# Kernel tuning notes

Measured on AMD Instinct MI355X. Metric: run time of the kernel, lower is better.

Reference implementation:

```python
import jax, jax.numpy as jnp
import numpy as np

B, T, U, H = 4, 256, 64, 512
INNER, VOCAB = 512, 1024


def setup_inputs() -> dict:
    key = jax.random.key(0)
    ks = jax.random.split(key, 6)
    s_in = 1.0 / np.sqrt(2 * H)
    s_h = 1.0 / np.sqrt(INNER)
    return {
        "enc_state": jax.random.normal(ks[0], (B, T, H), dtype=jnp.float32),
        "dec_state": jax.random.normal(ks[1], (B, U, H), dtype=jnp.float32),
        "W1": jax.random.normal(ks[2], (2 * H, INNER), dtype=jnp.float32) * s_in,
        "b1": jnp.zeros((INNER,), dtype=jnp.float32),
        "W2": jax.random.normal(ks[3], (INNER, VOCAB), dtype=jnp.float32) * s_h,
        "b2": jnp.zeros((VOCAB,), dtype=jnp.float32),
    }


def reference(enc_state, dec_state, W1, b1, W2, b2):
    # JointNet: broadcast enc [B,T,1,H] and dec [B,1,U,H], concat -> Linear -> tanh -> Linear -> log_softmax
    # concat+Linear is split into two smaller matmuls (mathematically identical):
    # cat([e,d]) @ W1 == e @ W1[:H] + d @ W1[H:]
    enc_proj = jnp.einsum("bth,hi->bti", enc_state, W1[:H])      # [B,T,INNER]
    dec_proj = jnp.einsum("buh,hi->bui", dec_state, W1[H:])      # [B,U,INNER]
    hidden = jnp.tanh(enc_proj[:, :, None, :] + dec_proj[:, None, :, :] + b1)  # [B,T,U,INNER]
    logits = jnp.einsum("btui,iv->btuv", hidden, W2) + b2        # [B,T,U,VOCAB]
    return jax.nn.log_softmax(logits, axis=-1)
```

## Files before the change

### kernel.cpp

```cpp
#include <hip/hip_runtime.h>
#include <hip/hip_bf16.h>
#include <cstdint>
#include <cstddef>


typedef __attribute__((ext_vector_type(4))) float f32x4;

#define BS_CHUNK 32768

#define WS_EP_OFF 0
#define WS_DP_OFF (1024 * 512 * 4)
#define WS_W2_OFF (WS_DP_OFF + 256 * 512 * 4)

#define ASTRIDE 528
#define LDS_EP 33792
#define LDS_B0 36864
#define LDS_B1 69632
#define SMEM_TOTAL 102400

__device__ __forceinline__ unsigned short f2bf(float x) {
  unsigned int u = __builtin_bit_cast(unsigned int, x);
  u += 0x7FFFu + ((u >> 16) & 1u);
  return (unsigned short)(u >> 16);
}

__device__ __forceinline__ float fast_tanh(float x) {
  float ax = fabsf(x);
  float e = __expf(-2.0f * ax);
  float t = (1.0f - e) * __builtin_amdgcn_rcpf(1.0f + e);
  return copysignf(t, x);
}

#if __has_builtin(__builtin_amdgcn_cvt_pk_fp8_f32)
__device__ __forceinline__ unsigned int f2fp8x4(float a, float b, float c, float d) {
  unsigned int w = 0;
  w = (unsigned int)__builtin_amdgcn_cvt_pk_fp8_f32(a, b, (int)w, false);
  w = (unsigned int)__builtin_amdgcn_cvt_pk_fp8_f32(c, d, (int)w, true);
  return w;
}
#else
__device__ __forceinline__ unsigned int enc_e4m3(float x) {
  unsigned int u = __builtin_bit_cast(unsigned int, x);
  unsigned int s = (u >> 24) & 0x80u;
  float ax = fabsf(x);
  if (!(ax < 448.0f)) return s | 0x7Eu;
  if (ax < 0.0009765625f) return s;
  int e; float fr = frexpf(ax, &e);
  int E = e + 6;
  if (E >= 1) {
    unsigned int m = (unsigned int)rintf(fr * 16.0f);
    if (m == 16u) { m = 8u; E += 1; }
    if (E >= 16) return s | 0x7Eu;
    return s | ((unsigned int)E << 3) | (m - 8u);
  } else {
    unsigned int m = (unsigned int)rintf(ax * 512.0f);
    if (m >= 8u) return s | 0x08u;
    return s | m;
  }
}
__device__ __forceinline__ unsigned int f2fp8x4(float a, float b, float c, float d) {
  return enc_e4m3(a) | (enc_e4m3(b) << 8) | (enc_e4m3(c) << 16) | (enc_e4m3(d) << 24);
}
#endif

__global__ __launch_bounds__(512) void prep(
    const float* __restrict__ enc, const float* __restrict__ dec,
    const float* __restrict__ W1, const float* __restrict__ b1,
    const float* __restrict__ W2,
    float* __restrict__ ep, float* __restrict__ dp, char* __restrict__ w8st) {
  __shared__ float As[8 * 512];
  const int tid = threadIdx.x;
  if (blockIdx.x < 160) {
    const int r0 = blockIdx.x * 8;
    const bool isenc = (r0 < 1024);
    const float* A = isenc ? (enc + (size_t)r0 * 512) : (dec + (size_t)(r0 - 1024) * 512);
    const float* W = isenc ? W1 : (W1 + 512 * 512);
    float* O = isenc ? (ep + (size_t)r0 * 512) : (dp + (size_t)(r0 - 1024) * 512);

    for (int idx = tid; idx < 8 * 512; idx += 512) As[idx] = A[idx];
    __syncthreads();

    const int c = tid;
    float acc[8];
#pragma unroll
    for (int r = 0; r < 8; ++r) acc[r] = 0.0f;
    const float4* As4 = (const float4*)As;
#pragma unroll 2
    for (int k4 = 0; k4 < 128; ++k4) {
      const int kb = k4 * 4;
      float w0 = W[(size_t)(kb + 0) * 512 + c];
      float w1 = W[(size_t)(kb + 1) * 512 + c];
      float w2 = W[(size_t)(kb + 2) * 512 + c];
      float w3 = W[(size_t)(kb + 3) * 512 + c];
#pragma unroll
      for (int r = 0; r < 8; ++r) {
        float4 a = As4[r * 128 + k4];
        acc[r] += a.x * w0 + a.y * w1 + a.z * w2 + a.w * w3;
      }
    }
    const float bias = isenc ? b1[c] : 0.0f;
#pragma unroll
    for (int r = 0; r < 8; ++r) O[(size_t)r * 512 + c] = acc[r] + bias;
  } else {
    const int g = (blockIdx.x - 160) * 512 + tid;
    const int v = g & 1023;
    const int kc = g >> 10;
    const int s = (v >> 2) & 3;
    unsigned long long* dst =
        (unsigned long long*)(w8st + (size_t)kc * BS_CHUNK + (size_t)v * 32);
#pragma unroll
    for (int q = 0; q < 4; ++q) {
      float f[8];
#pragma unroll
      for (int j = 0; j < 8; ++j)
        f[j] = W2[(size_t)(kc * 32 + q * 8 + j) * 1024 + v];
      unsigned int lo = f2fp8x4(f[0], f[1], f[2], f[3]);
      unsigned int hi = f2fp8x4(f[4], f[5], f[6], f[7]);
      dst[q ^ s] = (unsigned long long)lo | ((unsigned long long)hi << 32);
    }
  }
}

__device__ __forceinline__ void stage32(const char* __restrict__ src, char* dst,
                                        int wave, int lane) {
  const int off = wave * 2048 + lane * 16;
#pragma unroll
  for (int j = 0; j < 2; ++j)
    __builtin_amdgcn_global_load_lds(
        (const __attribute__((address_space(1))) unsigned int*)(src + off + j * 1024),
        (__attribute__((address_space(3))) unsigned int*)(dst + off + j * 1024), 16, 0, 0);
}

__global__ __launch_bounds__(1024, 4) void joint(
    const float* __restrict__ ep, const float* __restrict__ dp,
    const char* __restrict__ w8st, const float* __restrict__ b2,
    float* __restrict__ out) {
  extern __shared__ char smem[];
  char* Asm = smem;
  float* epL = (float*)(smem + LDS_EP);
  char* Bs0 = smem + LDS_B0;
  char* Bs1 = smem + LDS_B1;
  float* redM = (float*)(smem + LDS_B0);
  float* redF = redM + 1024;
  float* redS = redF + 64;
  float* redF2 = redS + 1024;

  const int tid = threadIdx.x;
  const int wave = tid >> 6, lane = tid & 63;
  const int lo = lane & 15, hi = lane >> 4;
  const int bt = blockIdx.x;
  const int m0 = bt * 64;
  const int dprow0 = (bt >> 8) * 64;
  const int nbase = wave * 64;
  const int krot = bt & 15;

  float b2v[4];
#pragma unroll
  for (int ni = 0; ni < 4; ++ni) b2v[ni] = b2[nbase + ni * 16 + lo];

  stage32(w8st + (size_t)krot * BS_CHUNK, Bs0, wave, lane);
  stage32(w8st + (size_t)((krot + 1) & 15) * BS_CHUNK, Bs1, wave, lane);

  if (tid < 128) ((float4*)epL)[tid] = ((const float4*)(ep + (size_t)bt * 512))[tid];

  const int arow = tid & 63;
  const int c0 = (tid >> 6) * 32;
  float d[32];
  {
    const float* dpr = dp + (size_t)(dprow0 + arow) * 512 + c0;
#pragma unroll
    for (int j = 0; j < 8; ++j) *(float4*)(d + j * 4) = ((const float4*)dpr)[j];
  }
  __syncthreads();

  {
    unsigned int w8[8];
#pragma unroll
    for (int q = 0; q < 8; ++q) {
      float h0 = fast_tanh(epL[c0 + q * 4 + 0] + d[q * 4 + 0]);
      float h1 = fast_tanh(epL[c0 + q * 4 + 1] + d[q * 4 + 1]);
      float h2 = fast_tanh(epL[c0 + q * 4 + 2] + d[q * 4 + 2]);
      float h3 = fast_tanh(epL[c0 + q * 4 + 3] + d[q * 4 + 3]);
      w8[q] = f2fp8x4(h0, h1, h2, h3);
    }
    uint4* aw = (uint4*)(Asm + arow * ASTRIDE + c0);
    aw[0] = *(const uint4*)(w8);
    aw[1] = *(const uint4*)(w8 + 4);
  }

  f32x4 acc[4][4];
#pragma unroll
  for (int mi = 0; mi < 4; ++mi)
#pragma unroll
    for (int ni = 0; ni < 4; ++ni)
#pragma unroll
      for (int j = 0; j < 4; ++j) acc[mi][ni][j] = 0.0f;

  asm volatile("s_waitcnt lgkmcnt(0)" ::: "memory");
  __builtin_amdgcn_s_barrier();
  __builtin_amdgcn_sched_barrier(0);

  const int bswz = (hi * 8) ^ (((lo >> 2) & 3) << 3);

#define K_ITER(I, RD)                                                            \
  {                                                                              \
    const int i_ = (I);                                                          \
    if (i_ >= 14) asm volatile("s_waitcnt vmcnt(0)" ::: "memory");               \
    else          asm volatile("s_waitcnt vmcnt(2)" ::: "memory");               \
    __builtin_amdgcn_s_barrier();             \
    __builtin_amdgcn_sched_barrier(0);                                           \
    const int gc = (i_ + krot) & 15;                                             \
    unsigned long long a[4], b[4];                                               \
    _Pragma("unroll")                                                            \
    for (int ni = 0; ni < 4; ++ni)                                               \
      b[ni] = *(const unsigned long long*)(RD + (size_t)(nbase + ni * 16 + lo) * 32 + bswz); \
    _Pragma("unroll")                                                            \
    for (int mi = 0; mi < 4; ++mi)                                               \
      a[mi] = *(const unsigned long long*)(Asm + (size_t)(mi * 16 + lo) * ASTRIDE + gc * 32 + hi * 8); \
    asm volatile("s_waitcnt lgkmcnt(0)" ::: "memory");                           \
    __builtin_amdgcn_sched_barrier(0);                                           \
    __builtin_amdgcn_s_barrier();                 \
    __builtin_amdgcn_sched_barrier(0);                                           \
    if (i_ < 14)                                                                 \
      stage32(w8st + (size_t)(((i_ + 2 + krot) & 15)) * BS_CHUNK, RD, wave, lane); \
    __builtin_amdgcn_s_setprio(1);                                               \
    _Pragma("unroll")                                                            \
    for (int ni = 0; ni < 4; ++ni)                                               \
      _Pragma("unroll")                                                          \
      for (int mi = 0; mi < 4; ++mi)                                             \
        acc[mi][ni] = __builtin_amdgcn_mfma_f32_16x16x32_fp8_fp8(                \
            (long)a[mi], (long)b[ni], acc[mi][ni], 0, 0, 0);                     \
    __builtin_amdgcn_s_setprio(0);                                               \
  }

#pragma unroll 1
  for (int i2 = 0; i2 < 8; ++i2) {
    K_ITER(i2 * 2, Bs0);
    K_ITER(i2 * 2 + 1, Bs1);
  }
#undef K_ITER

#pragma unroll
  for (int mi = 0; mi < 4; ++mi)
#pragma unroll
    for (int ni = 0; ni < 4; ++ni)
#pragma unroll
      for (int j = 0; j < 4; ++j) acc[mi][ni][j] += b2v[ni];

  float pm[4][4];
#pragma unroll
  for (int mi = 0; mi < 4; ++mi)
#pragma unroll
    for (int r = 0; r < 4; ++r)
      pm[mi][r] = fmaxf(fmaxf(acc[mi][0][r], acc[mi][1][r]),
                        fmaxf(acc[mi][2][r], acc[mi][3][r]));
#pragma unroll
  for (int off = 1; off < 16; off <<= 1)
#pragma unroll
    for (int mi = 0; mi < 4; ++mi)
#pragma unroll
      for (int r = 0; r < 4; ++r)
        pm[mi][r] = fmaxf(pm[mi][r], __shfl_xor(pm[mi][r], off));
  if (lo == 0) {
#pragma unroll
    for (int mi = 0; mi < 4; ++mi)
#pragma unroll
      for (int r = 0; r < 4; ++r)
        redM[wave * 64 + mi * 16 + hi * 4 + r] = pm[mi][r];
  }
  asm volatile("s_waitcnt lgkmcnt(0)" ::: "memory");
  __builtin_amdgcn_s_barrier();
  {
    const int rr = tid >> 4, w = tid & 15;
    float v = redM[w * 64 + rr];
#pragma unroll
    for (int off = 1; off < 16; off <<= 1) v = fmaxf(v, __shfl_xor(v, off));
    if (w == 0) redF[rr] = v;
  }
  asm volatile("s_waitcnt lgkmcnt(0)" ::: "memory");
  __builtin_amdgcn_s_barrier();
  float rm[4][4];
#pragma unroll
  for (int mi = 0; mi < 4; ++mi)
#pragma unroll
    for (int r = 0; r < 4; ++r) rm[mi][r] = redF[mi * 16 + hi * 4 + r];

  float ps[4][4];
#pragma unroll
  for (int mi = 0; mi < 4; ++mi)
#pragma unroll
    for (int r = 0; r < 4; ++r) {
      float s = 0.0f;
#pragma unroll
      for (int ni = 0; ni < 4; ++ni) s += __expf(acc[mi][ni][r] - rm[mi][r]);
      ps[mi][r] = s;
    }
#pragma unroll
  for (int off = 1; off < 16; off <<= 1)
#pragma unroll
    for (int mi = 0; mi < 4; ++mi)
#pragma unroll
      for (int r = 0; r < 4; ++r)
        ps[mi][r] += __shfl_xor(ps[mi][r], off);
  if (lo == 0) {
#pragma unroll
    for (int mi = 0; mi < 4; ++mi)
#pragma unroll
      for (int r = 0; r < 4; ++r)
        redS[wave * 64 + mi * 16 + hi * 4 + r] = ps[mi][r];
  }
  asm volatile("s_waitcnt lgkmcnt(0)" ::: "memory");
  __builtin_amdgcn_s_barrier();
  {
    const int rr = tid >> 4, w = tid & 15;
    float v = redS[w * 64 + rr];
#pragma unroll
    for (int off = 1; off < 16; off <<= 1) v += __shfl_xor(v, off);
    if (w == 0) redF2[rr] = v;
  }
  asm volatile("s_waitcnt lgkmcnt(0)" ::: "memory");
  __builtin_amdgcn_s_barrier();

#pragma unroll
  for (int mi = 0; mi < 4; ++mi)
#pragma unroll
    for (int r = 0; r < 4; ++r) {
      const int row = mi * 16 + hi * 4 + r;
      const float sub = rm[mi][r] + __logf(redF2[row]);
      float* op = out + (size_t)(m0 + row) * 1024 + nbase + lo;
#pragma unroll
      for (int ni = 0; ni < 4; ++ni) op[ni * 16] = acc[mi][ni][r] - sub;
    }
}

extern "C" void kernel_launch(void* const* d_in, const int* in_sizes, int n_in,
                              void* d_out, int out_size, void* d_ws, size_t ws_size,
                              hipStream_t stream) {
  const float* enc = (const float*)d_in[0];
  const float* dec = (const float*)d_in[1];
  const float* W1  = (const float*)d_in[2];
  const float* b1  = (const float*)d_in[3];
  const float* W2  = (const float*)d_in[4];
  const float* b2  = (const float*)d_in[5];
  float* out = (float*)d_out;

  char* ws = (char*)d_ws;
  float* ep = (float*)(ws + WS_EP_OFF);
  float* dp = (float*)(ws + WS_DP_OFF);
  char* w8st = ws + WS_W2_OFF;

  prep<<<192, 512, 0, stream>>>(enc, dec, W1, b1, W2, ep, dp, w8st);
  joint<<<1024, 1024, SMEM_TOTAL, stream>>>(ep, dp, w8st, b2, out);
}
```

Before: 208.7 us.

## Stage W2 per wave into private triple buffers to drop block barriers in K loop

```diff
diff --git a/kernel.cpp b/kernel.cpp
--- a/kernel.cpp
+++ b/kernel.cpp
@@ -13,10 +13,8 @@
 #define WS_W2_OFF (WS_DP_OFF + 256 * 512 * 4)
 
 #define ASTRIDE 528
-#define LDS_EP 33792
-#define LDS_B0 36864
-#define LDS_B1 69632
-#define SMEM_TOTAL 102400
+#define LDS_B 34816
+#define SMEM_TOTAL (34816 + 16 * 6144)
 
 __device__ __forceinline__ unsigned short f2bf(float x) {
   unsigned int u = __builtin_bit_cast(unsigned int, x);
@@ -105,7 +103,6 @@
     const int g = (blockIdx.x - 160) * 512 + tid;
     const int v = g & 1023;
     const int kc = g >> 10;
-    const int s = (v >> 2) & 3;
     unsigned long long* dst =
         (unsigned long long*)(w8st + (size_t)kc * BS_CHUNK + (size_t)v * 32);
 #pragma unroll
@@ -116,19 +113,20 @@
         f[j] = W2[(size_t)(kc * 32 + q * 8 + j) * 1024 + v];
       unsigned int lo = f2fp8x4(f[0], f[1], f[2], f[3]);
       unsigned int hi = f2fp8x4(f[4], f[5], f[6], f[7]);
-      dst[q ^ s] = (unsigned long long)lo | ((unsigned long long)hi << 32);
-    }
-  }
-}
-
-__device__ __forceinline__ void stage32(const char* __restrict__ src, char* dst,
-                                        int wave, int lane) {
-  const int off = wave * 2048 + lane * 16;
+      dst[q] = (unsigned long long)lo | ((unsigned long long)hi << 32);
+    }
+  }
+}
+
+__device__ __forceinline__ void stageW(const char* __restrict__ w8st, char* dst,
+                                       int gc, int nbase, int lane) {
+  const char* src = w8st + (size_t)gc * BS_CHUNK + (size_t)nbase * 32 + lane * 16;
 #pragma unroll
   for (int j = 0; j < 2; ++j)
     __builtin_amdgcn_global_load_lds(
-        (const __attribute__((address_space(1))) unsigned int*)(src + off + j * 1024),
-        (__attribute__((address_space(3))) unsigned int*)(dst + off + j * 1024), 16, 0, 0);
+        (const __attribute__((address_space(1))) unsigned int*)(src + j * 1024),
+        (__attribute__((address_space(3))) unsigned int*)(dst + j * 1024 + lane * 16),
+        16, 0, 0);
 }
 
 __global__ __launch_bounds__(1024, 4) void joint(
@@ -137,10 +135,7 @@
     float* __restrict__ out) {
   extern __shared__ char smem[];
   char* Asm = smem;
-  float* epL = (float*)(smem + LDS_EP);
-  char* Bs0 = smem + LDS_B0;
-  char* Bs1 = smem + LDS_B1;
-  float* redM = (float*)(smem + LDS_B0);
+  float* redM = (float*)smem;
   float* redF = redM + 1024;
   float* redS = redF + 64;
   float* redF2 = redS + 1024;
@@ -153,34 +148,34 @@
   const int dprow0 = (bt >> 8) * 64;
   const int nbase = wave * 64;
   const int krot = bt & 15;
-
-  float b2v[4];
-#pragma unroll
-  for (int ni = 0; ni < 4; ++ni) b2v[ni] = b2[nbase + ni * 16 + lo];
-
-  stage32(w8st + (size_t)krot * BS_CHUNK, Bs0, wave, lane);
-  stage32(w8st + (size_t)((krot + 1) & 15) * BS_CHUNK, Bs1, wave, lane);
-
-  if (tid < 128) ((float4*)epL)[tid] = ((const float4*)(ep + (size_t)bt * 512))[tid];
+  char* Bw = smem + LDS_B + wave * 6144;
 
   const int arow = tid & 63;
   const int c0 = (tid >> 6) * 32;
-  float d[32];
+  float ev[32], d[32];
   {
+    const float* epr = ep + (size_t)bt * 512 + c0;
     const float* dpr = dp + (size_t)(dprow0 + arow) * 512 + c0;
 #pragma unroll
+    for (int j = 0; j < 8; ++j) *(float4*)(ev + j * 4) = ((const float4*)epr)[j];
+#pragma unroll
     for (int j = 0; j < 8; ++j) *(float4*)(d + j * 4) = ((const float4*)dpr)[j];
   }
-  __syncthreads();
+  __builtin_amdgcn_sched_barrier(0);
+
+  stageW(w8st, Bw,        (krot) & 15,     nbase, lane);
+  stageW(w8st, Bw + 2048, (krot + 1) & 15, nbase, lane);
+  stageW(w8st, Bw + 4096, (krot + 2) & 15, nbase, lane);
+  __builtin_amdgcn_sched_barrier(0);
 
   {
     unsigned int w8[8];
 #pragma unroll
     for (int q = 0; q < 8; ++q) {
-      float h0 = fast_tanh(epL[c0 + q * 4 + 0] + d[q * 4 + 0]);
-      float h1 = fast_tanh(epL[c0 + q * 4 + 1] + d[q * 4 + 1]);
-      float h2 = fast_tanh(epL[c0 + q * 4 + 2] + d[q * 4 + 2]);
-      float h3 = fast_tanh(epL[c0 + q * 4 + 3] + d[q * 4 + 3]);
+      float h0 = fast_tanh(ev[q * 4 + 0] + d[q * 4 + 0]);
+      float h1 = fast_tanh(ev[q * 4 + 1] + d[q * 4 + 1]);
+      float h2 = fast_tanh(ev[q * 4 + 2] + d[q * 4 + 2]);
+      float h3 = fast_tanh(ev[q * 4 + 3] + d[q * 4 + 3]);
       w8[q] = f2fp8x4(h0, h1, h2, h3);
     }
     uint4* aw = (uint4*)(Asm + arow * ASTRIDE + c0);
@@ -200,52 +195,48 @@
   __builtin_amdgcn_s_barrier();
   __builtin_amdgcn_sched_barrier(0);
 
-  const int bswz = (hi * 8) ^ (((lo >> 2) & 3) << 3);
-
-#define K_ITER(I, RD)                                                            \
+#define K_IT(I, D)                                                               \
   {                                                                              \
-    const int i_ = (I);                                                          \
-    if (i_ >= 14) asm volatile("s_waitcnt vmcnt(0)" ::: "memory");               \
-    else          asm volatile("s_waitcnt vmcnt(2)" ::: "memory");               \
-    __builtin_amdgcn_s_barrier();             \
-    __builtin_amdgcn_sched_barrier(0);                                           \
-    const int gc = (i_ + krot) & 15;                                             \
-    unsigned long long a[4], b[4];                                               \
+    if ((I) <= 13)      asm volatile("s_waitcnt vmcnt(4)" ::: "memory");         \
+    else if ((I) == 14) asm volatile("s_waitcnt vmcnt(2)" ::: "memory");         \
+    else                asm volatile("s_waitcnt vmcnt(0)" ::: "memory");         \
+    const int gc_ = ((I) + krot) & 15;                                           \
+    unsigned long long a_[4], b_[4];                                             \
+    const char* bp_ = Bw + (D) * 2048;                                           \
     _Pragma("unroll")                                                            \
     for (int ni = 0; ni < 4; ++ni)                                               \
-      b[ni] = *(const unsigned long long*)(RD + (size_t)(nbase + ni * 16 + lo) * 32 + bswz); \
+      b_[ni] = *(const unsigned long long*)(bp_ + (ni * 16 + lo) * 32 + hi * 8); \
     _Pragma("unroll")                                                            \
     for (int mi = 0; mi < 4; ++mi)                                               \
-      a[mi] = *(const unsigned long long*)(Asm + (size_t)(mi * 16 + lo) * ASTRIDE + gc * 32 + hi * 8); \
+      a_[mi] = *(const unsigned long long*)(Asm + (mi * 16 + lo) * ASTRIDE + gc_ * 32 + hi * 8); \
     asm volatile("s_waitcnt lgkmcnt(0)" ::: "memory");                           \
     __builtin_amdgcn_sched_barrier(0);                                           \
-    __builtin_amdgcn_s_barrier();                 \
-    __builtin_amdgcn_sched_barrier(0);                                           \
-    if (i_ < 14)                                                                 \
-      stage32(w8st + (size_t)(((i_ + 2 + krot) & 15)) * BS_CHUNK, RD, wave, lane); \
-    __builtin_amdgcn_s_setprio(1);                                               \
+    if ((I) < 13) stageW(w8st, Bw + (D) * 2048, ((I) + 3 + krot) & 15, nbase, lane); \
     _Pragma("unroll")                                                            \
     for (int ni = 0; ni < 4; ++ni)                                               \
       _Pragma("unroll")                                                          \
       for (int mi = 0; mi < 4; ++mi)                                             \
         acc[mi][ni] = __builtin_amdgcn_mfma_f32_16x16x32_fp8_fp8(                \
-            (long)a[mi], (long)b[ni], acc[mi][ni], 0, 0, 0);                     \
-    __builtin_amdgcn_s_setprio(0);                                               \
-  }
-
-#pragma unroll 1
-  for (int i2 = 0; i2 < 8; ++i2) {
-    K_ITER(i2 * 2, Bs0);
-    K_ITER(i2 * 2 + 1, Bs1);
-  }
-#undef K_ITER
-
+            (long)a_[mi], (long)b_[ni], acc[mi][ni], 0, 0, 0);                   \
+  }
+
+  K_IT(0, 0)  K_IT(1, 1)  K_IT(2, 2)  K_IT(3, 0)
+  K_IT(4, 1)  K_IT(5, 2)  K_IT(6, 0)  K_IT(7, 1)
+  K_IT(8, 2)  K_IT(9, 0)  K_IT(10, 1) K_IT(11, 2)
+  K_IT(12, 0) K_IT(13, 1) K_IT(14, 2) K_IT(15, 0)
+#undef K_IT
+
+  float b2v[4];
+#pragma unroll
+  for (int ni = 0; ni < 4; ++ni) b2v[ni] = b2[nbase + ni * 16 + lo];
 #pragma unroll
   for (int mi = 0; mi < 4; ++mi)
 #pragma unroll
     for (int ni = 0; ni < 4; ++ni)
 #pragma unroll
       for (int j = 0; j < 4; ++j) acc[mi][ni][j] += b2v[ni];
+
+  __syncthreads();
 
   float pm[4][4];
 #pragma unroll
@@ -268,8 +259,7 @@
       for (int r = 0; r < 4; ++r)
         redM[wave * 64 + mi * 16 + hi * 4 + r] = pm[mi][r];
   }
-  asm volatile("s_waitcnt lgkmcnt(0)" ::: "memory");
-  __builtin_amdgcn_s_barrier();
+  __syncthreads();
   {
     const int rr = tid >> 4, w = tid & 15;
     float v = redM[w * 64 + rr];
@@ -277,8 +267,7 @@
     for (int off = 1; off < 16; off <<= 1) v = fmaxf(v, __shfl_xor(v, off));
     if (w == 0) redF[rr] = v;
   }
-  asm volatile("s_waitcnt lgkmcnt(0)" ::: "memory");
-  __builtin_amdgcn_s_barrier();
+  __syncthreads();
   float rm[4][4];
 #pragma unroll
   for (int mi = 0; mi < 4; ++mi)
@@ -309,8 +298,7 @@
       for (int r = 0; r < 4; ++r)
         redS[wave * 64 + mi * 16 + hi * 4 + r] = ps[mi][r];
   }
-  asm volatile("s_waitcnt lgkmcnt(0)" ::: "memory");
-  __builtin_amdgcn_s_barrier();
+  __syncthreads();
   {
     const int rr = tid >> 4, w = tid & 15;
     float v = redS[w * 64 + rr];
@@ -318,8 +306,7 @@
     for (int off = 1; off < 16; off <<= 1) v += __shfl_xor(v, off);
     if (w == 0) redF2[rr] = v;
   }
-  asm volatile("s_waitcnt lgkmcnt(0)" ::: "memory");
-  __builtin_amdgcn_s_barrier();
+  __syncthreads();
 
 #pragma unroll
   for (int mi = 0; mi < 4; ++mi)
```

New measurement: 193.3 us. -7.4%, faster.
